# Optimization experiments

Measured on AMD Instinct MI355X. Metric: run time of the kernel, lower is better.

Reference implementation:

```python
import jax, jax.numpy as jnp
import numpy as np

N_NODES = 100000
N_EDGES = 1600000
N_GRAPHS = 2048
IN0 = 33
H = 100
NUM_TASKS = 1
BN_EPS = 1e-5


def _gcn_layer(x, W, b, row, col, norm, n):
    # x: [N, Cin] -> [N, Cout]; GCNConv: symmetric-normalized aggregation of x @ W, plus bias
    xw = x @ W                                   # [N, Cout]
    msg = xw[row] * norm[:, None]                # [E+N, Cout] gathered + scaled messages
    out = jax.ops.segment_sum(msg, col, num_segments=n)
    return out + b


def _bn_eval(h, gamma, beta, mean, var):
    return (h - mean) * jax.lax.rsqrt(var + BN_EPS) * gamma + beta


def setup_inputs() -> dict:
    key = jax.random.key(0)
    ks = jax.random.split(key, 16)
    x = jax.random.normal(ks[0], (N_NODES, IN0), dtype=jnp.float32)
    edge_index = jax.random.randint(ks[1], (2, N_EDGES), 0, N_NODES, dtype=jnp.int64)
    batch = jnp.sort(jax.random.randint(ks[2], (N_NODES,), 0, N_GRAPHS, dtype=jnp.int64))
    # Xavier-uniform linear weights (as in _initialize_weights), zero biases
    def xav(k, fan_in, fan_out):
        lim = np.sqrt(6.0 / (fan_in + fan_out))
        return jax.random.uniform(k, (fan_in, fan_out), jnp.float32, -lim, lim)
    W0 = xav(ks[3], IN0, H)                      # layer 0: 33 -> 100
    Ws = jnp.stack([xav(ks[4 + i], H, H) for i in range(3)])  # layers 1..3: 100 -> 100
    biases = jnp.zeros((4, H), jnp.float32)
    gamma = 1.0 + 0.1 * jax.random.normal(ks[7], (4, H), jnp.float32)
    beta = 0.1 * jax.random.normal(ks[8], (4, H), jnp.float32)
    bn_mean = 0.1 * jax.random.normal(ks[9], (4, H), jnp.float32)
    bn_var = 1.0 + 0.1 * jax.random.uniform(ks[10], (4, H), jnp.float32)
    head_W = xav(ks[11], H, NUM_TASKS)
    head_b = jnp.zeros((NUM_TASKS,), jnp.float32)
    return {"x": x, "edge_index": edge_index, "batch": batch, "W0": W0, "Ws": Ws,
            "biases": biases, "gamma": gamma, "beta": beta, "bn_mean": bn_mean,
            "bn_var": bn_var, "head_W": head_W, "head_b": head_b}


def reference(x, edge_index, batch, W0, Ws, biases, gamma, beta, bn_mean, bn_var, head_W, head_b):
    n = x.shape[0]
    loop = jnp.arange(n, dtype=edge_index.dtype)
    row = jnp.concatenate([edge_index[0], loop])     # sources (+ self loops)
    col = jnp.concatenate([edge_index[1], loop])     # destinations (+ self loops)
    deg = jax.ops.segment_sum(jnp.ones_like(col, dtype=x.dtype), col, num_segments=n)
    dis = jnp.where(deg > 0, jax.lax.rsqrt(jnp.maximum(deg, 1.0)), 0.0)
    norm = dis[row] * dis[col]                       # [E+N] symmetric GCN normalization
    h = x
    for l in range(4):
        W = W0 if l == 0 else Ws[l - 1]
        h = _gcn_layer(h, W, biases[l], row, col, norm, n)
        h = _bn_eval(h, gamma[l], beta[l], bn_mean[l], bn_var[l])
        if l < 3:
            h = jax.nn.relu(h)
        # dropout: identity in eval mode
    g = jax.ops.segment_sum(h, batch, num_segments=N_GRAPHS)  # global_add_pool [G, H]
    out = g @ head_W + head_b
    return jnp.where(out >= 0, out, 0.1 * out)       # LeakyReLU(0.1)
```

## Files before the change

kernel.cpp:

```cpp
#include <hip/hip_runtime.h>
#include <hip/hip_fp16.h>

#define H100 100
#define BN_EPS 1e-5f
#define MAXD 64
#define CSR_CAP 5120
#define NB_MAX 1024

typedef _Float16 h2t __attribute__((ext_vector_type(2)));

__device__ __forceinline__ float dot2f(h2t a, h2t b, float c) {
#if defined(__has_builtin) && __has_builtin(__builtin_amdgcn_fdot2)
    return __builtin_amdgcn_fdot2(a, b, c, false);
#else
    return c + (float)a.x * (float)b.x + (float)a.y * (float)b.y;
#endif
}

__device__ __forceinline__ float4 h4tof4(const uint2 u) {
    const __half2 h0 = *reinterpret_cast<const __half2*>(&u.x);
    const __half2 h1 = *reinterpret_cast<const __half2*>(&u.y);
    const float2 f0 = __half22float2(h0);
    const float2 f1 = __half22float2(h1);
    return make_float4(f0.x, f0.y, f1.x, f1.y);
}
__device__ __forceinline__ uint2 f4toh4(const float4 v) {
    __half2 h0 = __float22half2_rn(make_float2(v.x, v.y));
    __half2 h1 = __float22half2_rn(make_float2(v.z, v.w));
    uint2 u;
    u.x = *reinterpret_cast<const unsigned int*>(&h0);
    u.y = *reinterpret_cast<const unsigned int*>(&h1);
    return u;
}
__device__ __forceinline__ void f4p(float4& a, const float4 b) {
    a.x += b.x; a.y += b.y; a.z += b.z; a.w += b.w;
}

__global__ __launch_bounds__(256) void init_kernel(
    const float* __restrict__ b, const float* __restrict__ gamma,
    const float* __restrict__ beta, const float* __restrict__ mean,
    const float* __restrict__ var, const float* __restrict__ W0,
    const float* __restrict__ Ws, const float* __restrict__ headW,
    float* __restrict__ sarr, float* __restrict__ tarr,
    h2t* __restrict__ W0p2, h2t* __restrict__ W1p2, h2t* __restrict__ W2p2,
    float* __restrict__ wp, float* __restrict__ c3,
    float* __restrict__ gacc, int G,
    int* __restrict__ bucketCnt, int NB)
{
    const int t = threadIdx.x;
    if (blockIdx.x == 0) {
        __shared__ float ws_[H100];
        const float* W3 = Ws + 2 * H100 * H100;
        for (int idx = t; idx < 4 * H100; idx += 256) {
            float s = gamma[idx] * rsqrtf(var[idx] + BN_EPS);
            sarr[idx] = s;
            tarr[idx] = (b[idx] - mean[idx]) * s + beta[idx];
        }
        __syncthreads();
        if (t < H100) ws_[t] = sarr[3 * H100 + t] * headW[t];
        __syncthreads();
        if (t < H100) {
            float acc = 0.f;
            for (int c = 0; c < H100; ++c) acc += W3[t * H100 + c] * ws_[c];
            wp[t] = acc;
        }
        if (t == 0) {
            float acc = 0.f;
            for (int c = 0; c < H100; ++c) acc += tarr[3 * H100 + c] * headW[c];
            *c3 = acc;
        }
        return;
    }
    int idx = (blockIdx.x - 1) * 256 + t;
    if (idx < 1800) {
        int k2 = idx / 100, c = idx - k2 * 100;
        int k0 = 2 * k2, k1 = 2 * k2 + 1;
        float v0 = (k0 < 33) ? W0[k0 * H100 + c] : 0.f;
        float v1 = (k1 < 33) ? W0[k1 * H100 + c] : 0.f;
        h2t p; p.x = (_Float16)v0; p.y = (_Float16)v1;
        W0p2[idx] = p;
    } else if (idx < 6800) {
        int j = idx - 1800;
        int k2 = j / 100, c = j - k2 * 100;
        h2t p;
        p.x = (_Float16)Ws[(2 * k2) * H100 + c];
        p.y = (_Float16)Ws[(2 * k2 + 1) * H100 + c];
        W1p2[j] = p;
    } else if (idx < 12000) {
        int j = idx - 6800;
        int k2 = j / 104, c = j - k2 * 104;
        const float* W2 = Ws + H100 * H100;
        h2t p; p.x = (_Float16)0.f; p.y = (_Float16)0.f;
        if (c < H100) {
            p.x = (_Float16)W2[(2 * k2) * H100 + c];
            p.y = (_Float16)W2[(2 * k2 + 1) * H100 + c];
        }
        W2p2[j] = p;
    } else {
        int g = idx - 12000;
        if (g < G) gacc[g] = 0.f;
        else if (g - G < NB) bucketCnt[g - G] = 0;
    }
}

__global__ __launch_bounds__(512) void csr_p1_kernel(
    const int* __restrict__ row, const int* __restrict__ col,
    int* __restrict__ bucketCnt, unsigned int* __restrict__ bucketBuf,
    int E, int NB)
{
    __shared__ int hcnt[NB_MAX];
    __shared__ int hbase[NB_MAX];
    const int tid = threadIdx.x;
    for (int j = tid; j < NB; j += 512) hcnt[j] = 0;
    __syncthreads();

    const int e0 = blockIdx.x * 4096 + tid;
    int bk[8], rk[8];
    unsigned int pv[8];
    bool v[8];
    #pragma unroll
    for (int k = 0; k < 8; ++k) {
        const int e = e0 + k * 512;
        v[k] = (e < E);
        const int c = v[k] ? col[e] : 0;
        const int r = v[k] ? row[e] : 0;
        bk[k] = c >> 8;
        pv[k] = (unsigned int)r | ((unsigned int)(c & 255) << 24);
        if (v[k]) rk[k] = atomicAdd(&hcnt[bk[k]], 1);
    }
    __syncthreads();
    for (int j = tid; j < NB; j += 512)
        if (hcnt[j] > 0) hbase[j] = atomicAdd(&bucketCnt[j], hcnt[j]);
    __syncthreads();
    #pragma unroll
    for (int k = 0; k < 8; ++k) {
        if (v[k]) {
            const int pos = hbase[bk[k]] + rk[k];
            if (pos < CSR_CAP)
                bucketBuf[(size_t)bk[k] * CSR_CAP + pos] = pv[k];
        }
    }
}

__global__ __launch_bounds__(512) void csr_p2_kernel(
    const int* __restrict__ bucketCnt, const unsigned int* __restrict__ bucketBuf,
    int* __restrict__ cnt, float* __restrict__ dis, int* __restrict__ srcidx,
    int n)
{
    __shared__ int lcnt[256];
    const int b = blockIdx.x;
    const int tid = threadIdx.x;
    if (tid < 256) lcnt[tid] = 0;
    __syncthreads();
    const int cb = min(bucketCnt[b], CSR_CAP);
    const unsigned int* __restrict__ bp = bucketBuf + (size_t)b * CSR_CAP;
    const int node0 = b << 8;
    for (int pos = tid; pos < cb; pos += 512) {
        const unsigned int v = bp[pos];
        const int d = (int)(v >> 24);
        const int r = (int)(v & 0xFFFFFFu);
        const int s = atomicAdd(&lcnt[d], 1);
        if (s < MAXD) srcidx[(size_t)(node0 + d) * MAXD + s] = r;
    }
    __syncthreads();
    if (tid < 256) {
        const int node = node0 + tid;
        if (node < n) {
            const int c = lcnt[tid];
            cnt[node] = c;
            dis[node] = rsqrtf((float)(c + 1));
        }
    }
}

__global__ __launch_bounds__(256) void xpad_kernel(
    const float* __restrict__ x, const float* __restrict__ dis,
    uint2* __restrict__ xts, int n)
{
    int tt = blockIdx.x * 256 + threadIdx.x;
    int node = tt / 9;
    if (node >= n) return;
    int q = tt - node * 9;
    const float dn = dis[node];
    float v[4];
    #pragma unroll
    for (int j = 0; j < 4; ++j) {
        int c = q * 4 + j;
        v[j] = (c < 33) ? x[node * 33 + c] * dn : 0.f;
    }
    xts[node * 9 + q] = f4toh4(make_float4(v[0], v[1], v[2], v[3]));
}

__global__ __launch_bounds__(256) void gather33_kernel(
    const int* __restrict__ cnt, const int* __restrict__ srcidx,
    const uint2* __restrict__ xts, const float* __restrict__ dis,
    uint2* __restrict__ agg0h, int n)
{
    const int t = blockIdx.x * 256 + threadIdx.x;
    const int node = t / 9;
    if (node >= n) return;
    const int q = t - node * 9;
    const float dn = dis[node];
    const int* __restrict__ sp = srcidx + (size_t)node * MAXD;
    const int kd = min(cnt[node], MAXD);

    float4 a0 = h4tof4(xts[node * 9 + q]);
    float4 a1 = make_float4(0.f, 0.f, 0.f, 0.f);
    int i = 0;
    for (; i + 3 < kd; i += 4) {
        const uint2 u0 = xts[sp[i] * 9 + q];
        const uint2 u1 = xts[sp[i + 1] * 9 + q];
        const uint2 u2 = xts[sp[i + 2] * 9 + q];
        const uint2 u3 = xts[sp[i + 3] * 9 + q];
        f4p(a0, h4tof4(u0)); f4p(a1, h4tof4(u1));
        f4p(a0, h4tof4(u2)); f4p(a1, h4tof4(u3));
    }
    for (; i < kd; ++i) f4p(a1, h4tof4(xts[sp[i] * 9 + q]));
    agg0h[node * 9 + q] = f4toh4(make_float4(
        (a0.x + a1.x) * dn, (a0.y + a1.y) * dn, (a0.z + a1.z) * dn, (a0.w + a1.w) * dn));
}

__global__ __launch_bounds__(256) void gemm_fused36_kernel(
    const h2t* __restrict__ agg0h,
    const h2t* __restrict__ W0p2, const h2t* __restrict__ W1p2,
    const float* __restrict__ dis,
    const float* __restrict__ sarr0, const float* __restrict__ tarr0,
    uint2* __restrict__ z1h, int n)
{
    __shared__ h2t Wl[50 * H100];
    __shared__ h2t Uh[50 * 68];
    const int tid = threadIdx.x;
    const int node0 = blockIdx.x * 64;

    for (int idx = tid; idx < 64 * 18; idx += 256) {
        int r = idx / 18;
        int k2 = idx - r * 18;
        int node = node0 + r;
        h2t p; p.x = (_Float16)0.f; p.y = (_Float16)0.f;
        if (node < n) p = agg0h[node * 18 + k2];
        Uh[k2 * 68 + r] = p;
    }
    for (int idx = tid; idx < 450; idx += 256)
        reinterpret_cast<uint4*>(Wl)[idx] = reinterpret_cast<const uint4*>(W0p2)[idx];
    __syncthreads();

    const int tx = tid & 15;
    const int ty = tid >> 4;
    float acc0[4][4] = {{0.f}};
    float acc1[4][4] = {{0.f}};

    #pragma unroll 3
    for (int k2 = 0; k2 < 18; ++k2) {
        const uint4 av = *reinterpret_cast<const uint4*>(&Uh[k2 * 68 + ty * 4]);
        const h2t* a2 = reinterpret_cast<const h2t*>(&av);
        const uint4 w0v = *reinterpret_cast<const uint4*>(&Wl[k2 * H100 + tx * 4]);
        const h2t* w0 = reinterpret_cast<const h2t*>(&w0v);
        #pragma unroll
        for (int ni = 0; ni < 4; ++ni)
            #pragma unroll
            for (int ci = 0; ci < 4; ++ci)
                acc0[ni][ci] = dot2f(a2[ni], w0[ci], acc0[ni][ci]);
        if (tx < 9) {
            const uint4 w1v = *reinterpret_cast<const uint4*>(&Wl[k2 * H100 + 64 + tx * 4]);
            const h2t* w1 = reinterpret_cast<const h2t*>(&w1v);
            #pragma unroll
            for (int ni = 0; ni < 4; ++ni)
                #pragma unroll
                for (int ci = 0; ci < 4; ++ci)
                    acc1[ni][ci] = dot2f(a2[ni], w1[ci], acc1[ni][ci]);
        }
    }
    __syncthreads();

    {
        const float4 s0 = *reinterpret_cast<const float4*>(&sarr0[tx * 4]);
        const float4 t0 = *reinterpret_cast<const float4*>(&tarr0[tx * 4]);
        #pragma unroll
        for (int ni = 0; ni < 4; ++ni) {
            const int r = ty * 4 + ni;
            float h0 = fmaxf(acc0[ni][0] * s0.x + t0.x, 0.f);
            float h1 = fmaxf(acc0[ni][1] * s0.y + t0.y, 0.f);
            float hh2 = fmaxf(acc0[ni][2] * s0.z + t0.z, 0.f);
            float h3 = fmaxf(acc0[ni][3] * s0.w + t0.w, 0.f);
            h2t p0; p0.x = (_Float16)h0; p0.y = (_Float16)h1;
            h2t p1; p1.x = (_Float16)hh2; p1.y = (_Float16)h3;
            Uh[(tx * 2) * 68 + r] = p0;
            Uh[(tx * 2 + 1) * 68 + r] = p1;
        }
        if (tx < 9) {
            const float4 s1 = *reinterpret_cast<const float4*>(&sarr0[64 + tx * 4]);
            const float4 t1 = *reinterpret_cast<const float4*>(&tarr0[64 + tx * 4]);
            #pragma unroll
            for (int ni = 0; ni < 4; ++ni) {
                const int r = ty * 4 + ni;
                float h0 = fmaxf(acc1[ni][0] * s1.x + t1.x, 0.f);
                float h1 = fmaxf(acc1[ni][1] * s1.y + t1.y, 0.f);
                float hh2 = fmaxf(acc1[ni][2] * s1.z + t1.z, 0.f);
                float h3 = fmaxf(acc1[ni][3] * s1.w + t1.w, 0.f);
                h2t p0; p0.x = (_Float16)h0; p0.y = (_Float16)h1;
                h2t p1; p1.x = (_Float16)hh2; p1.y = (_Float16)h3;
                Uh[(32 + tx * 2) * 68 + r] = p0;
                Uh[(32 + tx * 2 + 1) * 68 + r] = p1;
            }
        }
    }
    for (int idx = tid; idx < 1250; idx += 256)
        reinterpret_cast<uint4*>(Wl)[idx] = reinterpret_cast<const uint4*>(W1p2)[idx];
    __syncthreads();

    float bcc0[4][4] = {{0.f}};
    float bcc1[4][4] = {{0.f}};
    #pragma unroll 5
    for (int k2 = 0; k2 < 50; ++k2) {
        const uint4 av = *reinterpret_cast<const uint4*>(&Uh[k2 * 68 + ty * 4]);
        const h2t* a2 = reinterpret_cast<const h2t*>(&av);
        const uint4 w0v = *reinterpret_cast<const uint4*>(&Wl[k2 * H100 + tx * 4]);
        const h2t* w0 = reinterpret_cast<const h2t*>(&w0v);
        #pragma unroll
        for (int ni = 0; ni < 4; ++ni)
            #pragma unroll
            for (int ci = 0; ci < 4; ++ci)
                bcc0[ni][ci] = dot2f(a2[ni], w0[ci], bcc0[ni][ci]);
        if (tx < 9) {
            const uint4 w1v = *reinterpret_cast<const uint4*>(&Wl[k2 * H100 + 64 + tx * 4]);
            const h2t* w1 = reinterpret_cast<const h2t*>(&w1v);
            #pragma unroll
            for (int ni = 0; ni < 4; ++ni)
                #pragma unroll
                for (int ci = 0; ci < 4; ++ci)
                    bcc1[ni][ci] = dot2f(a2[ni], w1[ci], bcc1[ni][ci]);
        }
    }

    #pragma unroll
    for (int ni = 0; ni < 4; ++ni) {
        const int node = node0 + ty * 4 + ni;
        if (node >= n) continue;
        const float d = dis[node];
        z1h[node * 25 + tx] = f4toh4(make_float4(
            bcc0[ni][0] * d, bcc0[ni][1] * d, bcc0[ni][2] * d, bcc0[ni][3] * d));
        if (tx < 9)
            z1h[node * 25 + 16 + tx] = f4toh4(make_float4(
                bcc1[ni][0] * d, bcc1[ni][1] * d, bcc1[ni][2] * d, bcc1[ni][3] * d));
    }
}

__global__ __launch_bounds__(512) void gather_gemm_kernel(
    const int* __restrict__ cnt, const int* __restrict__ srcidx,
    const uint2* __restrict__ z4, const float* __restrict__ dis,
    const float* __restrict__ sarr, const float* __restrict__ tarr,
    const h2t* __restrict__ W2p2, uint2* __restrict__ z2h, int n)
{
    __shared__ h2t Wl[50 * 104];
    __shared__ h2t hrow[20 * 52];
    const int tid = threadIdx.x;

    const int g = tid / 25;
    const int q = tid - g * 25;
    const bool act = (g < 20);
    const int node = blockIdx.x * 20 + g;
    const bool valid = act && (node < n);

    float4 a0 = make_float4(0.f, 0.f, 0.f, 0.f);
    float4 a1 = make_float4(0.f, 0.f, 0.f, 0.f);
    float dn = 0.f;
    if (valid) {
        a0 = h4tof4(z4[node * 25 + q]);
        dn = dis[node];
        const int* __restrict__ sp = srcidx + (size_t)node * MAXD;
        const int kd = min(cnt[node], MAXD);
        int i = 0;
        for (; i + 7 < kd; i += 8) {
            const uint2 u0 = z4[sp[i] * 25 + q];
            const uint2 u1 = z4[sp[i + 1] * 25 + q];
            const uint2 u2 = z4[sp[i + 2] * 25 + q];
            const uint2 u3 = z4[sp[i + 3] * 25 + q];
            const uint2 u4 = z4[sp[i + 4] * 25 + q];
            const uint2 u5 = z4[sp[i + 5] * 25 + q];
            const uint2 u6 = z4[sp[i + 6] * 25 + q];
            const uint2 u7 = z4[sp[i + 7] * 25 + q];
            f4p(a0, h4tof4(u0)); f4p(a1, h4tof4(u1));
            f4p(a0, h4tof4(u2)); f4p(a1, h4tof4(u3));
            f4p(a0, h4tof4(u4)); f4p(a1, h4tof4(u5));
            f4p(a0, h4tof4(u6)); f4p(a1, h4tof4(u7));
        }
        for (; i + 3 < kd; i += 4) {
            const uint2 u0 = z4[sp[i] * 25 + q];
            const uint2 u1 = z4[sp[i + 1] * 25 + q];
            const uint2 u2 = z4[sp[i + 2] * 25 + q];
            const uint2 u3 = z4[sp[i + 3] * 25 + q];
            f4p(a0, h4tof4(u0)); f4p(a1, h4tof4(u1));
            f4p(a0, h4tof4(u2)); f4p(a1, h4tof4(u3));
        }
        for (; i < kd; ++i) f4p(a1, h4tof4(z4[sp[i] * 25 + q]));
    }

    if (act) {
        const float4 s  = *reinterpret_cast<const float4*>(&sarr[q * 4]);
        const float4 tt = *reinterpret_cast<const float4*>(&tarr[q * 4]);
        float h0 = fmaxf((a0.x + a1.x) * dn * s.x + tt.x, 0.f);
        float h1 = fmaxf((a0.y + a1.y) * dn * s.y + tt.y, 0.f);
        float hh2 = fmaxf((a0.z + a1.z) * dn * s.z + tt.z, 0.f);
        float h3 = fmaxf((a0.w + a1.w) * dn * s.w + tt.w, 0.f);
        h2t p0; p0.x = (_Float16)h0; p0.y = (_Float16)h1;
        h2t p1; p1.x = (_Float16)hh2; p1.y = (_Float16)h3;
        hrow[g * 52 + q * 2]     = p0;
        hrow[g * 52 + q * 2 + 1] = p1;
    }

    for (int idx = tid; idx < 1300; idx += 512)
        reinterpret_cast<uint4*>(Wl)[idx] = reinterpret_cast<const uint4*>(W2p2)[idx];
    __syncthreads();

    if (valid) {
        float z0 = 0.f, zz1 = 0.f, z2v = 0.f, z3 = 0.f;
        const h2t* hp = &hrow[g * 52];
        #pragma unroll 5
        for (int k2 = 0; k2 < 50; ++k2) {
            const uint4 wv = *reinterpret_cast<const uint4*>(&Wl[k2 * 104 + q * 4]);
            const h2t* wh = reinterpret_cast<const h2t*>(&wv);
            const h2t hv = hp[k2];
            z0  = dot2f(hv, wh[0], z0);
            zz1 = dot2f(hv, wh[1], zz1);
            z2v = dot2f(hv, wh[2], z2v);
            z3  = dot2f(hv, wh[3], z3);
        }
        z2h[node * 25 + q] = f4toh4(make_float4(z0 * dn, zz1 * dn, z2v * dn, z3 * dn));
    }
}

__global__ __launch_bounds__(256) void gather100_head_kernel(
    const int* __restrict__ cnt, const int* __restrict__ srcidx,
    const uint2* __restrict__ z4, const float* __restrict__ dis,
    const float* __restrict__ sarr, const float* __restrict__ tarr,
    const float* __restrict__ wp, float* __restrict__ y, int n)
{
    const int tid = threadIdx.x;
    const int node = blockIdx.x * 10 + tid / 25;
    const int q = tid % 25;
    const bool valid = (tid < 250) && (node < n);

    float4 a0 = make_float4(0.f, 0.f, 0.f, 0.f);
    float4 a1 = make_float4(0.f, 0.f, 0.f, 0.f);
    float dn = 0.f;
    if (valid) {
        a0 = h4tof4(z4[node * 25 + q]);
        dn = dis[node];
        const int* __restrict__ sp = srcidx + (size_t)node * MAXD;
        const int kd = min(cnt[node], MAXD);
        int i = 0;
        for (; i + 7 < kd; i += 8) {
            const uint2 u0 = z4[sp[i] * 25 + q];
            const uint2 u1 = z4[sp[i + 1] * 25 + q];
            const uint2 u2 = z4[sp[i + 2] * 25 + q];
            const uint2 u3 = z4[sp[i + 3] * 25 + q];
            const uint2 u4 = z4[sp[i + 4] * 25 + q];
            const uint2 u5 = z4[sp[i + 5] * 25 + q];
            const uint2 u6 = z4[sp[i + 6] * 25 + q];
            const uint2 u7 = z4[sp[i + 7] * 25 + q];
            f4p(a0, h4tof4(u0)); f4p(a1, h4tof4(u1));
            f4p(a0, h4tof4(u2)); f4p(a1, h4tof4(u3));
            f4p(a0, h4tof4(u4)); f4p(a1, h4tof4(u5));
            f4p(a0, h4tof4(u6)); f4p(a1, h4tof4(u7));
        }
        for (; i + 3 < kd; i += 4) {
            const uint2 u0 = z4[sp[i] * 25 + q];
            const uint2 u1 = z4[sp[i + 1] * 25 + q];
            const uint2 u2 = z4[sp[i + 2] * 25 + q];
            const uint2 u3 = z4[sp[i + 3] * 25 + q];
            f4p(a0, h4tof4(u0)); f4p(a1, h4tof4(u1));
            f4p(a0, h4tof4(u2)); f4p(a1, h4tof4(u3));
        }
        for (; i < kd; ++i) f4p(a1, h4tof4(z4[sp[i] * 25 + q]));
    }

    const float4 s  = *reinterpret_cast<const float4*>(&sarr[q * 4]);
    const float4 tt = *reinterpret_cast<const float4*>(&tarr[q * 4]);
    const float4 w  = *reinterpret_cast<const float4*>(&wp[q * 4]);
    float hv0 = fmaxf((a0.x + a1.x) * dn * s.x + tt.x, 0.f);
    float hv1 = fmaxf((a0.y + a1.y) * dn * s.y + tt.y, 0.f);
    float hv2 = fmaxf((a0.z + a1.z) * dn * s.z + tt.z, 0.f);
    float hv3 = fmaxf((a0.w + a1.w) * dn * s.w + tt.w, 0.f);
    float partial = hv0 * w.x + hv1 * w.y + hv2 * w.z + hv3 * w.w;

    __shared__ float red[256];
    red[tid] = valid ? partial : 0.f;
    __syncthreads();
    if (valid && q == 0) {
        float sum = 0.f;
        #pragma unroll
        for (int j = 0; j < 25; ++j) sum += red[tid + j];
        y[node] = sum * dn;
    }
}

__global__ __launch_bounds__(256) void gather_scalar_kernel(
    const int* __restrict__ cnt, const int* __restrict__ srcidx,
    const float* __restrict__ y, const float* __restrict__ dis,
    const float* __restrict__ c3, const int* __restrict__ batch,
    float* __restrict__ gacc, int n)
{
    const int node = blockIdx.x * 256 + threadIdx.x;
    if (node >= n) return;
    float acc = y[node];
    float accb = 0.f;
    const int* __restrict__ sp = srcidx + (size_t)node * MAXD;
    const int kd = min(cnt[node], MAXD);
    int i = 0;
    for (; i + 7 < kd; i += 8) {
        acc  += (y[sp[i]]     + y[sp[i + 1]]) + (y[sp[i + 2]] + y[sp[i + 3]]);
        accb += (y[sp[i + 4]] + y[sp[i + 5]]) + (y[sp[i + 6]] + y[sp[i + 7]]);
    }
    for (; i + 3 < kd; i += 4)
        acc += (y[sp[i]] + y[sp[i + 1]]) + (y[sp[i + 2]] + y[sp[i + 3]]);
    for (; i < kd; ++i) acc += y[sp[i]];
    unsafeAtomicAdd(&gacc[batch[node]], dis[node] * (acc + accb) + c3[0]);
}

__global__ __launch_bounds__(256) void finish_kernel(const float* __restrict__ gacc,
                                                     const float* __restrict__ hb,
                                                     float* __restrict__ out, int G) {
    int g = blockIdx.x * 256 + threadIdx.x;
    if (g >= G) return;
    float o = gacc[g] + hb[0];
    out[g] = (o >= 0.f) ? o : 0.1f * o;
}

extern "C" void kernel_launch(void* const* d_in, const int* in_sizes, int n_in,
                              void* d_out, int out_size, void* d_ws, size_t ws_size,
                              hipStream_t stream) {
    const float* x       = (const float*)d_in[0];
    const int*   ei      = (const int*)d_in[1];
    const int*   batch   = (const int*)d_in[2];
    const float* W0      = (const float*)d_in[3];
    const float* Ws      = (const float*)d_in[4];
    const float* biases  = (const float*)d_in[5];
    const float* gamma   = (const float*)d_in[6];
    const float* beta    = (const float*)d_in[7];
    const float* bn_mean = (const float*)d_in[8];
    const float* bn_var  = (const float*)d_in[9];
    const float* headW   = (const float*)d_in[10];
    const float* headb   = (const float*)d_in[11];
    float* out = (float*)d_out;

    const int N = in_sizes[2];
    const int E = in_sizes[1] / 2;
    const int G = out_size;
    const int* row  = ei;
    const int* colp = ei + E;

    char* ws = (char*)d_ws;
    size_t off = 0;
    auto carve = [&](size_t bytes) -> void* {
        void* p = (void*)(ws + off);
        off += (bytes + 255) & ~(size_t)255;
        return p;
    };
    float*  dis    = (float*)carve((size_t)N * 4);
    uint2*  xts    = (uint2*)carve((size_t)N * 9 * 8);
    uint2*  agg0h  = (uint2*)carve((size_t)N * 9 * 8);
    uint2*  bufA   = (uint2*)carve((size_t)N * 25 * 8);
    uint2*  bufB   = (uint2*)carve((size_t)N * 25 * 8);
    float*  y      = (float*)carve((size_t)N * 4);
    int*    cnt    = (int*)carve((size_t)N * 4);
    int*    srcidx = (int*)carve((size_t)N * MAXD * 4);
    float*  sarr   = (float*)carve(4 * H100 * 4);
    float*  tarr   = (float*)carve(4 * H100 * 4);
    float*  wp     = (float*)carve(H100 * 4);
    float*  c3     = (float*)carve(256);
    h2t*    W0p2   = (h2t*)carve(1800 * 4);
    h2t*    W1p2   = (h2t*)carve(5000 * 4);
    h2t*    W2p2   = (h2t*)carve(5200 * 4);
    float*  gacc   = (float*)carve((size_t)G * 4);

    const int NB = (N + 255) >> 8;
    unsigned int* bucketBuf = (unsigned int*)carve((size_t)NB * CSR_CAP * 4);
    int*          bucketCnt = (int*)carve((size_t)NB * 4);

    const int nb_n   = (N + 255) / 256;
    const int nb_g   = (N + 63) / 64;
    const int nb_9   = (N * 9 + 255) / 256;
    const int nb_ga  = (N + 9) / 10;
    const int nb_gg  = (N + 19) / 20;
    const int nb_p1  = (E + 4095) / 4096;
    const int nb_pad = (12000 + G + NB + 255) / 256;

    init_kernel<<<1 + nb_pad, 256, 0, stream>>>(
        biases, gamma, beta, bn_mean, bn_var, W0,
        Ws, headW, sarr, tarr, W0p2, W1p2, W2p2, wp, c3, gacc, G, bucketCnt, NB);

    csr_p1_kernel<<<nb_p1, 512, 0, stream>>>(row, colp, bucketCnt, bucketBuf, E, NB);
    csr_p2_kernel<<<NB, 512, 0, stream>>>(bucketCnt, bucketBuf, cnt, dis, srcidx, N);

    xpad_kernel<<<nb_9, 256, 0, stream>>>(x, dis, xts, N);

    gather33_kernel<<<nb_9, 256, 0, stream>>>(cnt, srcidx, xts, dis, agg0h, N);
    gemm_fused36_kernel<<<nb_g, 256, 0, stream>>>((const h2t*)agg0h, W0p2, W1p2, dis,
                                                  sarr, tarr, bufA, N);

    gather_gemm_kernel<<<nb_gg, 512, 0, stream>>>(cnt, srcidx, bufA, dis,
                                                  sarr + H100, tarr + H100,
                                                  W2p2, bufB, N);

    gather100_head_kernel<<<nb_ga, 256, 0, stream>>>(cnt, srcidx, bufB, dis,
                                                     sarr + 2 * H100, tarr + 2 * H100, wp, y, N);

    gather_scalar_kernel<<<nb_n, 256, 0, stream>>>(cnt, srcidx, y, dis, c3, batch, gacc, N);
    finish_kernel<<<(G + 255) / 256, 256, 0, stream>>>(gacc, headb, out, G);
}
```

Measured before the change: 382.4 us.

## Fuse xpad into CSR pass and layer-0 gather into first GEMM

Folds the x scaling and fp16 packing into the CSR second-pass kernel, using a shared-memory copy of the degree normalization. It also moves the 33-wide neighbor gather into the fused GEMM kernel, writing results straight into shared memory. This removes two launches and the agg0h round trip through global memory. The cost is that the GEMM kernel now carries the irregular gather latency in its prologue, with only 576 work items spread over 256 threads.

```diff
diff --git a/kernel.cpp b/kernel.cpp
--- a/kernel.cpp
+++ b/kernel.cpp
@@ -145,9 +145,10 @@
 __global__ __launch_bounds__(512) void csr_p2_kernel(
     const int* __restrict__ bucketCnt, const unsigned int* __restrict__ bucketBuf,
     int* __restrict__ cnt, float* __restrict__ dis, int* __restrict__ srcidx,
-    int n)
+    const float* __restrict__ x, uint2* __restrict__ xts, int n)
 {
     __shared__ int lcnt[256];
+    __shared__ float ldis[256];
     const int b = blockIdx.x;
     const int tid = threadIdx.x;
     if (tid < 256) lcnt[tid] = 0;
@@ -168,60 +169,31 @@
         if (node < n) {
             const int c = lcnt[tid];
             cnt[node] = c;
-            dis[node] = rsqrtf((float)(c + 1));
-        }
-    }
-}
-
-__global__ __launch_bounds__(256) void xpad_kernel(
-    const float* __restrict__ x, const float* __restrict__ dis,
-    uint2* __restrict__ xts, int n)
-{
-    int tt = blockIdx.x * 256 + threadIdx.x;
-    int node = tt / 9;
-    if (node >= n) return;
-    int q = tt - node * 9;
-    const float dn = dis[node];
-    float v[4];
-    #pragma unroll
-    for (int j = 0; j < 4; ++j) {
-        int c = q * 4 + j;
-        v[j] = (c < 33) ? x[node * 33 + c] * dn : 0.f;
-    }
-    xts[node * 9 + q] = f4toh4(make_float4(v[0], v[1], v[2], v[3]));
-}
-
-__global__ __launch_bounds__(256) void gather33_kernel(
+            const float d = rsqrtf((float)(c + 1));
+            dis[node] = d;
+            ldis[tid] = d;
+        }
+    }
+    __syncthreads();
+    for (int idx = tid; idx < 256 * 9; idx += 512) {
+        const int r = idx / 9;
+        const int q = idx - r * 9;
+        const int node = node0 + r;
+        if (node >= n) continue;
+        const float dn = ldis[r];
+        float v[4];
+        #pragma unroll
+        for (int j = 0; j < 4; ++j) {
+            const int c = q * 4 + j;
+            v[j] = (c < 33) ? x[node * 33 + c] * dn : 0.f;
+        }
+        xts[node * 9 + q] = f4toh4(make_float4(v[0], v[1], v[2], v[3]));
+    }
+}
+
+__global__ __launch_bounds__(256) void gemm_fused36_kernel(
     const int* __restrict__ cnt, const int* __restrict__ srcidx,
-    const uint2* __restrict__ xts, const float* __restrict__ dis,
-    uint2* __restrict__ agg0h, int n)
-{
-    const int t = blockIdx.x * 256 + threadIdx.x;
-    const int node = t / 9;
-    if (node >= n) return;
-    const int q = t - node * 9;
-    const float dn = dis[node];
-    const int* __restrict__ sp = srcidx + (size_t)node * MAXD;
-    const int kd = min(cnt[node], MAXD);
-
-    float4 a0 = h4tof4(xts[node * 9 + q]);
-    float4 a1 = make_float4(0.f, 0.f, 0.f, 0.f);
-    int i = 0;
-    for (; i + 3 < kd; i += 4) {
-        const uint2 u0 = xts[sp[i] * 9 + q];
-        const uint2 u1 = xts[sp[i + 1] * 9 + q];
-        const uint2 u2 = xts[sp[i + 2] * 9 + q];
-        const uint2 u3 = xts[sp[i + 3] * 9 + q];
-        f4p(a0, h4tof4(u0)); f4p(a1, h4tof4(u1));
-        f4p(a0, h4tof4(u2)); f4p(a1, h4tof4(u3));
-    }
-    for (; i < kd; ++i) f4p(a1, h4tof4(xts[sp[i] * 9 + q]));
-    agg0h[node * 9 + q] = f4toh4(make_float4(
-        (a0.x + a1.x) * dn, (a0.y + a1.y) * dn, (a0.z + a1.z) * dn, (a0.w + a1.w) * dn));
-}
-
-__global__ __launch_bounds__(256) void gemm_fused36_kernel(
-    const h2t* __restrict__ agg0h,
+    const uint2* __restrict__ xts,
     const h2t* __restrict__ W0p2, const h2t* __restrict__ W1p2,
     const float* __restrict__ dis,
     const float* __restrict__ sarr0, const float* __restrict__ tarr0,
@@ -232,16 +204,40 @@
     const int tid = threadIdx.x;
     const int node0 = blockIdx.x * 64;
 
-    for (int idx = tid; idx < 64 * 18; idx += 256) {
-        int r = idx / 18;
-        int k2 = idx - r * 18;
-        int node = node0 + r;
-        h2t p; p.x = (_Float16)0.f; p.y = (_Float16)0.f;
-        if (node < n) p = agg0h[node * 18 + k2];
-        Uh[k2 * 68 + r] = p;
-    }
     for (int idx = tid; idx < 450; idx += 256)
         reinterpret_cast<uint4*>(Wl)[idx] = reinterpret_cast<const uint4*>(W0p2)[idx];
+
+    for (int idx = tid; idx < 576; idx += 256) {
+        const int r = idx / 9;
+        const int q = idx - r * 9;
+        const int node = node0 + r;
+        float4 a0 = make_float4(0.f, 0.f, 0.f, 0.f);
+        float4 a1 = a0;
+        float dn = 0.f;
+        if (node < n) {
+            a0 = h4tof4(xts[node * 9 + q]);
+            dn = dis[node];
+            const int* __restrict__ sp = srcidx + (size_t)node * MAXD;
+            const int kd = min(cnt[node], MAXD);
+            int i = 0;
+            for (; i + 3 < kd; i += 4) {
+                const uint2 u0 = xts[sp[i] * 9 + q];
+                const uint2 u1 = xts[sp[i + 1] * 9 + q];
+                const uint2 u2 = xts[sp[i + 2] * 9 + q];
+                const uint2 u3 = xts[sp[i + 3] * 9 + q];
+                f4p(a0, h4tof4(u0)); f4p(a1, h4tof4(u1));
+                f4p(a0, h4tof4(u2)); f4p(a1, h4tof4(u3));
+            }
+            for (; i < kd; ++i) f4p(a0, h4tof4(xts[sp[i] * 9 + q]));
+        }
+        const uint2 p = f4toh4(make_float4(
+            (a0.x + a1.x) * dn, (a0.y + a1.y) * dn, (a0.z + a1.z) * dn, (a0.w + a1.w) * dn));
+        h2t plo, phi;
+        plo = *reinterpret_cast<const h2t*>(&p.x);
+        phi = *reinterpret_cast<const h2t*>(&p.y);
+        Uh[(2 * q) * 68 + r] = plo;
+        Uh[(2 * q + 1) * 68 + r] = phi;
+    }
     __syncthreads();
 
     const int tx = tid & 15;
@@ -558,7 +554,6 @@
     };
     float*  dis    = (float*)carve((size_t)N * 4);
     uint2*  xts    = (uint2*)carve((size_t)N * 9 * 8);
-    uint2*  agg0h  = (uint2*)carve((size_t)N * 9 * 8);
     uint2*  bufA   = (uint2*)carve((size_t)N * 25 * 8);
     uint2*  bufB   = (uint2*)carve((size_t)N * 25 * 8);
     float*  y      = (float*)carve((size_t)N * 4);
@@ -579,7 +574,6 @@
 
     const int nb_n   = (N + 255) / 256;
     const int nb_g   = (N + 63) / 64;
-    const int nb_9   = (N * 9 + 255) / 256;
     const int nb_ga  = (N + 9) / 10;
     const int nb_gg  = (N + 19) / 20;
     const int nb_p1  = (E + 4095) / 4096;
@@ -590,12 +584,10 @@
         Ws, headW, sarr, tarr, W0p2, W1p2, W2p2, wp, c3, gacc, G, bucketCnt, NB);
 
     csr_p1_kernel<<<nb_p1, 512, 0, stream>>>(row, colp, bucketCnt, bucketBuf, E, NB);
-    csr_p2_kernel<<<NB, 512, 0, stream>>>(bucketCnt, bucketBuf, cnt, dis, srcidx, N);
-
-    xpad_kernel<<<nb_9, 256, 0, stream>>>(x, dis, xts, N);
-
-    gather33_kernel<<<nb_9, 256, 0, stream>>>(cnt, srcidx, xts, dis, agg0h, N);
-    gemm_fused36_kernel<<<nb_g, 256, 0, stream>>>((const h2t*)agg0h, W0p2, W1p2, dis,
+    csr_p2_kernel<<<NB, 512, 0, stream>>>(bucketCnt, bucketBuf, cnt, dis, srcidx,
+                                          x, xts, N);
+
+    gemm_fused36_kernel<<<nb_g, 256, 0, stream>>>(cnt, srcidx, xts, W0p2, W1p2, dis,
                                                   sarr, tarr, bufA, N);
 
     gather_gemm_kernel<<<nb_gg, 512, 0, stream>>>(cnt, srcidx, bufA, dis,
```

After: 383.0 us. About the same (+0.1%).
